# Kernel optimization log

Hardware: AMD Instinct MI355X
Metric: run time of the kernel (lower is better)

Reference implementation:

```python
import jax, jax.numpy as jnp
import numpy as np
from jax import lax

FH, FW = 38, 63          # feature map H,W (600x1000 image, stride 16)
A = 9                    # anchors per location (3 scales x 3 ratios)
POOL = 7                 # cfg.POOLING_SIZE
PRE_NMS, POST_NMS = 6000, 300
NMS_THRESH = 0.7
IM_H, IM_W = 600.0, 1000.0
STRIDE = 16.0


def _make_anchors(h, w, stride=16):
    ratios = np.array([0.5, 1.0, 2.0]); scales = np.array([8.0, 16.0, 32.0])
    base = 16.0; ctr = (base - 1.0) / 2.0
    ws = np.round(np.sqrt(base * base / ratios)); hs = np.round(ws * ratios)
    ws = (ws[:, None] * scales[None, :]).ravel(); hs = (hs[:, None] * scales[None, :]).ravel()
    ba = np.stack([ctr - 0.5 * (ws - 1), ctr - 0.5 * (hs - 1),
                   ctr + 0.5 * (ws - 1), ctr + 0.5 * (hs - 1)], 1)
    sx, sy = np.meshgrid(np.arange(w) * stride, np.arange(h) * stride)
    shifts = np.stack([sx.ravel(), sy.ravel(), sx.ravel(), sy.ravel()], 1)
    return (shifts[:, None, :] + ba[None]).reshape(-1, 4).astype(np.float32)


def _conv(x, w, b, pad):
    y = lax.conv_general_dilated(x, w, (1, 1), pad,
                                 dimension_numbers=('NCHW', 'OIHW', 'NCHW'))
    return y + b[None, :, None, None]


def _bbox_transform_inv(anchors, deltas):
    w = anchors[:, 2] - anchors[:, 0] + 1.0
    h = anchors[:, 3] - anchors[:, 1] + 1.0
    cx = anchors[:, 0] + 0.5 * w
    cy = anchors[:, 1] + 0.5 * h
    dx, dy, dw, dh = deltas[:, 0], deltas[:, 1], deltas[:, 2], deltas[:, 3]
    pcx = dx * w + cx; pcy = dy * h + cy
    pw = jnp.exp(dw) * w; ph = jnp.exp(dh) * h
    return jnp.stack([pcx - 0.5 * pw, pcy - 0.5 * ph,
                      pcx + 0.5 * pw, pcy + 0.5 * ph], 1)


def _nms_keep(boxes, thresh):
    # greedy NMS over score-sorted boxes, fixed-size keep mask
    x1, y1, x2, y2 = boxes[:, 0], boxes[:, 1], boxes[:, 2], boxes[:, 3]
    areas = (x2 - x1 + 1.0) * (y2 - y1 + 1.0)
    iw = jnp.maximum(jnp.minimum(x2[:, None], x2[None, :])
                     - jnp.maximum(x1[:, None], x1[None, :]) + 1.0, 0.0)
    ih = jnp.maximum(jnp.minimum(y2[:, None], y2[None, :])
                     - jnp.maximum(y1[:, None], y1[None, :]) + 1.0, 0.0)
    inter = iw * ih
    iou = inter / (areas[:, None] + areas[None, :] - inter)
    n = boxes.shape[0]; ar = jnp.arange(n)
    def body(i, keep):
        sup = (iou[i] > thresh) & (ar > i) & keep[i]
        return keep & ~sup
    return lax.fori_loop(0, n, body, jnp.ones((n,), bool))


def _crop_and_resize(feat, boxes, crop):
    # feat [C,H,W]; boxes [R,4] normalized (y1,x1,y2,x2); TF crop_and_resize semantics
    C, H, W = feat.shape
    t = jnp.arange(crop, dtype=feat.dtype) / (crop - 1)
    def one(box):
        by1, bx1, by2, bx2 = box
        ys = by1 * (H - 1) + t * (by2 - by1) * (H - 1)
        xs = bx1 * (W - 1) + t * (bx2 - bx1) * (W - 1)
        y0f = jnp.floor(ys); x0f = jnp.floor(xs)
        wy = (ys - y0f)[None, :, None]; wx = (xs - x0f)[None, None, :]
        y0 = jnp.clip(y0f, 0, H - 1).astype(jnp.int32)
        y1i = jnp.clip(y0f + 1, 0, H - 1).astype(jnp.int32)
        x0 = jnp.clip(x0f, 0, W - 1).astype(jnp.int32)
        x1i = jnp.clip(x0f + 1, 0, W - 1).astype(jnp.int32)
        f00 = feat[:, y0][:, :, x0]; f01 = feat[:, y0][:, :, x1i]
        f10 = feat[:, y1i][:, :, x0]; f11 = feat[:, y1i][:, :, x1i]
        return (f00 * (1 - wy) * (1 - wx) + f01 * (1 - wy) * wx
                + f10 * wy * (1 - wx) + f11 * wy * wx)
    return jax.vmap(one)(boxes)


def _forward(net_conv, w_rpn, b_rpn, w_cls, b_cls, w_bbox, b_bbox, anchors):
    # _region_proposal: 3x3 rpn conv + relu, 1x1 cls / bbox heads
    rpn = jax.nn.relu(_conv(net_conv, w_rpn, b_rpn, 'SAME'))
    cls = _conv(rpn, w_cls, b_cls, 'VALID')    # [1,2A,H,W]
    bbox = _conv(rpn, w_bbox, b_bbox, 'VALID')  # [1,4A,H,W]
    # view(1,2,-1,W) softmax: channel a pairs with channel a+A (bg/fg)
    bg, fg = cls[:, :A], cls[:, A:]
    fg_prob = jax.nn.softmax(jnp.stack([bg, fg], axis=1), axis=1)[:, 1]  # [1,A,H,W]
    scores = jnp.transpose(fg_prob, (0, 2, 3, 1)).reshape(-1)            # (H*W*A,)
    deltas = jnp.transpose(bbox, (0, 2, 3, 1)).reshape(-1, 4)
    proposals = _bbox_transform_inv(anchors, deltas)
    proposals = jnp.stack([jnp.clip(proposals[:, 0], 0.0, IM_W - 1.0),
                           jnp.clip(proposals[:, 1], 0.0, IM_H - 1.0),
                           jnp.clip(proposals[:, 2], 0.0, IM_W - 1.0),
                           jnp.clip(proposals[:, 3], 0.0, IM_H - 1.0)], 1)
    # proposal selection is non-differentiable (rois.detach() in original)
    scores_sg = lax.stop_gradient(scores)
    props_sg = lax.stop_gradient(proposals)
    _, order = lax.top_k(scores_sg, PRE_NMS)
    boxes = props_sg[order]
    keep = _nms_keep(boxes, NMS_THRESH)
    idx = jnp.sort(jnp.where(keep, jnp.arange(PRE_NMS), PRE_NMS))[:POST_NMS]
    rois = boxes[jnp.minimum(idx, PRE_NMS - 1)]  # [300,4] (x1,y1,x2,y2)
    # _crop_pool_layer with max_pool=True: crop to 14x14 then 2x2 max pool
    H, W = net_conv.shape[2], net_conv.shape[3]
    x1 = rois[:, 0] / STRIDE; y1 = rois[:, 1] / STRIDE
    x2 = rois[:, 2] / STRIDE; y2 = rois[:, 3] / STRIDE
    norm = jnp.stack([y1 / (H - 1), x1 / (W - 1), y2 / (H - 1), x2 / (W - 1)], 1)
    crops = _crop_and_resize(net_conv[0], norm, 2 * POOL)  # [300,C,14,14]
    R, C = crops.shape[0], crops.shape[1]
    return crops.reshape(R, C, POOL, 2, POOL, 2).max(axis=(3, 5))  # [300,C,7,7]


def setup_inputs():
    key = jax.random.key(0)
    ks = jax.random.split(key, 4)
    net_conv = jax.random.normal(ks[0], (1, 512, FH, FW), jnp.float32)
    w_rpn = jax.random.normal(ks[1], (512, 512, 3, 3), jnp.float32) * 0.01
    b_rpn = jnp.zeros((512,), jnp.float32)
    w_cls = jax.random.normal(ks[2], (2 * A, 512, 1, 1), jnp.float32) * 0.01
    b_cls = jnp.zeros((2 * A,), jnp.float32)
    w_bbox = jax.random.normal(ks[3], (4 * A, 512, 1, 1), jnp.float32) * 0.01
    b_bbox = jnp.zeros((4 * A,), jnp.float32)
    anchors = jnp.asarray(_make_anchors(FH, FW))
    return {"net_conv": net_conv, "w_rpn": w_rpn, "b_rpn": b_rpn,
            "w_cls": w_cls, "b_cls": b_cls, "w_bbox": w_bbox,
            "b_bbox": b_bbox, "anchors": anchors}


def reference(net_conv, w_rpn, b_rpn, w_cls, b_cls, w_bbox, b_bbox, anchors):
    return _forward(net_conv, w_rpn, b_rpn, w_cls, b_cls, w_bbox, b_bbox, anchors)
```

## Files before the change

kernel.cpp:

```cpp
#include <hip/hip_runtime.h>
#include <stdint.h>

#define NPOS 2394
#define CIN 512
#define KK 4608
#define NANCH 21546
#define PRE 6000
#define POST 300
#define NWORD 94
#define NQ 8
#define QLEN 2694
#define FEATT_BYTES 4902912

#define OFF_BH    0
#define OFF_BL    4718592
#define OFF_P0    9437184
#define OFF_SBOX  9437184
#define OFF_KEEP  9533440
#define OFF_P1    14340096
#define OFF_KEYS  19243008
#define OFF_PROP  19415552
#define OFF_RPART 19760384
#define OFF_FPH   20450048
#define OFF_FPL   23179264

typedef _Float16 half8 __attribute__((ext_vector_type(8)));
typedef float f32x4 __attribute__((ext_vector_type(4)));

__device__ __forceinline__ void gload16(const void* g, void* l) {
    __builtin_amdgcn_global_load_lds((const __attribute__((address_space(1))) void*)g,
                                     (__attribute__((address_space(3))) void*)l, 16, 0, 0);
}

__global__ __launch_bounds__(256) void k_transpose_feat(const float* __restrict__ in,
                                                        float* __restrict__ featT) {
    __shared__ float tl[32][33];
    int tx = threadIdx.x & 31, tg = threadIdx.x >> 5;
    int posBase = blockIdx.x * 32, ciBase = blockIdx.y * 32;
#pragma unroll
    for (int j = 0; j < 4; ++j) {
        int ci = ciBase + tg + j * 8;
        int pos = posBase + tx;
        tl[tg + j * 8][tx] = (pos < NPOS) ? in[(size_t)ci * NPOS + pos] : 0.f;
    }
    __syncthreads();
#pragma unroll
    for (int j = 0; j < 4; ++j) {
        int pos = posBase + tg + j * 8;
        int ci = ciBase + tx;
        if (pos < NPOS) featT[(size_t)pos * 512 + ci] = tl[tx][tg + j * 8];
    }
}

__global__ void k_pad_split(const float* __restrict__ featT,
                            _Float16* __restrict__ FPH, _Float16* __restrict__ FPL) {
    int idx = blockIdx.x * 256 + threadIdx.x;
    int ci = idx & 511;
    int rc = idx >> 9;
    int hp = rc / 65, wp = rc - hp * 65;
    int h = hp - 1, w = wp - 1;
    float a = 0.f;
    if ((unsigned)h < 38u && (unsigned)w < 63u)
        a = featT[(size_t)(h * 63 + w) * 512 + ci] * 16.f;
    _Float16 ah = (_Float16)a;
    _Float16 al = (_Float16)(a - (float)ah);
    FPH[idx] = ah; FPL[idx] = al;
}

__global__ void k_prep_wf16(const float* __restrict__ w,
                            _Float16* __restrict__ BH, _Float16* __restrict__ BL) {
    int idx = blockIdx.x * 256 + threadIdx.x;
    int co = idx / KK;
    int rem = idx - co * KK;
    int p = rem >> 9;
    int ci = rem & 511;
    float b = w[(co * CIN + ci) * 9 + p] * 128.f;
    _Float16 bh = (_Float16)b;
    _Float16 bl = (_Float16)(b - (float)bh);
    BH[idx] = bh; BL[idx] = bl;
}

__global__ __launch_bounds__(256, 3) void k_conv3_mfma(
    const _Float16* __restrict__ FPH, const _Float16* __restrict__ FPL,
    const _Float16* __restrict__ BHp, const _Float16* __restrict__ BLp,
    float* __restrict__ P0, float* __restrict__ P1)
{
    __shared__ __align__(16) char lds[49152];
    const int t = threadIdx.x;
    const int wave = t >> 6, lane = t & 63;
    const int posBase = blockIdx.x * 128;
    const int coBase  = blockIdx.y * 64;
    const int z = blockIdx.z;
    float* __restrict__ P = z ? P1 : P0;
    const int wm = wave >> 1, wn = wave & 1;
    const int lr = lane & 15, lg = lane >> 4;

    int addrA[4][2], addrB[2][2];
#pragma unroll
    for (int m = 0; m < 4; ++m) {
        int row = wm * 64 + m * 16 + lr;
        int x = row & 7;
        addrA[m][0] = row * 128 + ((lg ^ x) << 4);
        addrA[m][1] = row * 128 + (((4 + lg) ^ x) << 4);
    }
#pragma unroll
    for (int n = 0; n < 2; ++n) {
        int row = wn * 32 + n * 16 + lr;
        int x = row & 7;
        addrB[n][0] = 32768 + row * 128 + ((lg ^ x) << 4);
        addrB[n][1] = 32768 + row * 128 + (((4 + lg) ^ x) << 4);
    }

    int baseA[4], ldsAo[4];
#pragma unroll
    for (int s = 0; s < 4; ++s) {
        int row = (wave * 4 + s) * 8 + (lane >> 3);
        int pos = posBase + row;
        int h = pos / 63;
        int w = pos - h * 63;
        int swz = ((lane & 7) ^ (row & 7)) * 8;
        baseA[s] = (h * 65 + w) * 512 + swz;
        ldsAo[s] = (wave * 4 + s) * 1024 + lane * 16;
    }
    int baseB[2], ldsBo[2];
#pragma unroll
    for (int s = 0; s < 2; ++s) {
        int row = (wave * 2 + s) * 8 + (lane >> 3);
        int swz = ((lane & 7) ^ (row & 7)) * 8;
        baseB[s] = (coBase + row) * KK + swz;
        ldsBo[s] = 32768 + (wave * 2 + s) * 1024 + lane * 16;
    }

    f32x4 acc[4][2];
#pragma unroll
    for (int m = 0; m < 4; ++m)
#pragma unroll
        for (int n = 0; n < 2; ++n) acc[m][n] = (f32x4){0.f, 0.f, 0.f, 0.f};

    const int kbeg = z * 2304;
    for (int step = 0; step < 36; ++step) {
        int k0 = kbeg + step * 64;
        int p = k0 >> 9;
        int ci0 = k0 & 511;
        int kh = p / 3;
        int kw = p - kh * 3;
        int dA = (kh * 65 + kw) * 512 + ci0;
#pragma unroll
        for (int s = 0; s < 4; ++s) {
            int so = baseA[s] + dA;
            gload16(FPH + so, lds + ldsAo[s]);
            gload16(FPL + so, lds + 16384 + ldsAo[s]);
        }
#pragma unroll
        for (int s = 0; s < 2; ++s) {
            int so = baseB[s] + k0;
            gload16(BHp + so, lds + ldsBo[s]);
            gload16(BLp + so, lds + 8192 + ldsBo[s]);
        }
        __syncthreads();
#pragma unroll
        for (int ks = 0; ks < 2; ++ks) {
            half8 aH[4], aL[4], bH[2], bL[2];
#pragma unroll
            for (int m = 0; m < 4; ++m) {
                aH[m] = *(const half8*)(lds + addrA[m][ks]);
                aL[m] = *(const half8*)(lds + 16384 + addrA[m][ks]);
            }
#pragma unroll
            for (int n = 0; n < 2; ++n) {
                bH[n] = *(const half8*)(lds + addrB[n][ks]);
                bL[n] = *(const half8*)(lds + 8192 + addrB[n][ks]);
            }
#pragma unroll
            for (int m = 0; m < 4; ++m)
#pragma unroll
                for (int n = 0; n < 2; ++n) {
                    acc[m][n] = __builtin_amdgcn_mfma_f32_16x16x32_f16(aH[m], bH[n], acc[m][n], 0, 0, 0);
                    acc[m][n] = __builtin_amdgcn_mfma_f32_16x16x32_f16(aH[m], bL[n], acc[m][n], 0, 0, 0);
                    acc[m][n] = __builtin_amdgcn_mfma_f32_16x16x32_f16(aL[m], bH[n], acc[m][n], 0, 0, 0);
                }
        }
        __syncthreads();
    }

#pragma unroll
    for (int m = 0; m < 4; ++m) {
        int pbase = posBase + wm * 64 + m * 16 + lg * 4;
        int co = coBase + wn * 32 + lr;
#pragma unroll
        for (int r = 0; r < 4; ++r) {
            int pos = pbase + r;
            if (pos < NPOS) {
                P[(size_t)pos * 512 + co]      = acc[m][0][r] * (1.f / 2048.f);
                P[(size_t)pos * 512 + co + 16] = acc[m][1][r] * (1.f / 2048.f);
            }
        }
    }
}

__global__ __launch_bounds__(256) void k_heads(const float* __restrict__ P0,
                                               const float* __restrict__ P1,
                                               const float* __restrict__ brpn,
                                               const float* __restrict__ wcls,
                                               const float* __restrict__ bcls,
                                               const float* __restrict__ wbbox,
                                               const float* __restrict__ bbbox,
                                               const float* __restrict__ anchors,
                                               float* __restrict__ proposals,
                                               unsigned long long* __restrict__ keys) {
    __shared__ float x[512];
    __shared__ float part[54][4];
    __shared__ float logit[54];
    int pos = blockIdx.x;
    int t = threadIdx.x;
    {
        float v0 = P0[(size_t)pos * 512 + t] + P1[(size_t)pos * 512 + t] + brpn[t];
        float v1 = P0[(size_t)pos * 512 + t + 256] + P1[(size_t)pos * 512 + t + 256] + brpn[t + 256];
        x[t] = v0 > 0.f ? v0 : 0.f;
        x[t + 256] = v1 > 0.f ? v1 : 0.f;
    }
    __syncthreads();
    if (t < 216) {
        int o = t >> 2, q = t & 3;
        const float* wr = (o < 18) ? (wcls + o * 512) : (wbbox + (o - 18) * 512);
        float s = 0.f;
        int base = q * 128;
#pragma unroll 4
        for (int k2 = 0; k2 < 128; ++k2) s += x[base + k2] * wr[base + k2];
        part[o][q] = s;
    }
    __syncthreads();
    if (t < 54) {
        float b = (t < 18) ? bcls[t] : bbbox[t - 18];
        logit[t] = part[t][0] + part[t][1] + part[t][2] + part[t][3] + b;
    }
    __syncthreads();
    if (t < 9) {
        int a = t;
        float bg = logit[a], fg = logit[9 + a];
        float score = 1.f / (1.f + expf(bg - fg));
        float dx = logit[18 + 4 * a], dy = logit[19 + 4 * a];
        float dw = logit[20 + 4 * a], dh = logit[21 + 4 * a];
        int idx = pos * 9 + a;
        float ax1 = anchors[idx * 4 + 0], ay1 = anchors[idx * 4 + 1];
        float ax2 = anchors[idx * 4 + 2], ay2 = anchors[idx * 4 + 3];
        float aw = ax2 - ax1 + 1.f, ah = ay2 - ay1 + 1.f;
        float cx = ax1 + 0.5f * aw, cy = ay1 + 0.5f * ah;
        float pcx = dx * aw + cx, pcy = dy * ah + cy;
        float pw = expf(dw) * aw, ph = expf(dh) * ah;
        float x1 = fminf(fmaxf(pcx - 0.5f * pw, 0.f), 999.f);
        float y1 = fminf(fmaxf(pcy - 0.5f * ph, 0.f), 599.f);
        float x2 = fminf(fmaxf(pcx + 0.5f * pw, 0.f), 999.f);
        float y2 = fminf(fmaxf(pcy + 0.5f * ph, 0.f), 599.f);
        proposals[idx * 4 + 0] = x1; proposals[idx * 4 + 1] = y1;
        proposals[idx * 4 + 2] = x2; proposals[idx * 4 + 3] = y2;
        union { float f; unsigned int i; } sv; sv.f = score;
        keys[idx] = (((unsigned long long)sv.i) << 32) |
                    (unsigned long long)(0xFFFFFFFFu - (unsigned)idx);
    }
}

__global__ __launch_bounds__(256) void k_rank_partial(const unsigned long long* __restrict__ keys,
                                                      unsigned int* __restrict__ rpart) {
    __shared__ unsigned long long kc[1024];
    int i = blockIdx.x * 256 + threadIdx.x;
    int q = blockIdx.y;
    unsigned long long myk = (i < NANCH) ? keys[i] : 0xFFFFFFFFFFFFFFFFull;
    int j0 = q * QLEN;
    int j1 = j0 + QLEN; if (j1 > NANCH) j1 = NANCH;
    unsigned int cnt = 0;
    for (int base = j0; base < j1; base += 1024) {
        int nload = j1 - base; if (nload > 1024) nload = 1024;
        __syncthreads();
        for (int u = threadIdx.x; u < 1024; u += 256)
            kc[u] = (base + u < j1) ? keys[base + u] : 0ull;
        __syncthreads();
        for (int u = 0; u < nload; ++u)
            cnt += (kc[u] > myk) ? 1u : 0u;
    }
    if (i < NANCH) rpart[i * NQ + q] = cnt;
}

__global__ void k_zero_sboxes(float* __restrict__ sboxes) {
    int i = blockIdx.x * 256 + threadIdx.x;
    if (i < PRE * 4) sboxes[i] = 0.f;
}

__global__ void k_rank_scatter(const unsigned int* __restrict__ rpart,
                               const float* __restrict__ proposals,
                               float* __restrict__ sboxes) {
    int i = blockIdx.x * 256 + threadIdx.x;
    if (i >= NANCH) return;
    unsigned int r = 0;
#pragma unroll
    for (int q = 0; q < NQ; q++) r += rpart[i * NQ + q];
    if (r < PRE) {
        sboxes[r * 4 + 0] = proposals[i * 4 + 0];
        sboxes[r * 4 + 1] = proposals[i * 4 + 1];
        sboxes[r * 4 + 2] = proposals[i * 4 + 2];
        sboxes[r * 4 + 3] = proposals[i * 4 + 3];
    }
}

__global__ __launch_bounds__(64) void k_nms_mask(const float* __restrict__ sboxes,
                                                 unsigned long long* __restrict__ mask) {
    __shared__ float bx[64][4];
    int ib = blockIdx.x, jb = blockIdx.y;
    int lane = threadIdx.x;
    int j = jb * 64 + lane;
    if (j < PRE) {
        bx[lane][0] = sboxes[j * 4 + 0]; bx[lane][1] = sboxes[j * 4 + 1];
        bx[lane][2] = sboxes[j * 4 + 2]; bx[lane][3] = sboxes[j * 4 + 3];
    } else {
        bx[lane][0] = 3e8f; bx[lane][1] = 3e8f; bx[lane][2] = 3e8f; bx[lane][3] = 3e8f;
    }
    __syncthreads();
    int i = ib * 64 + lane;
    if (i >= PRE) return;
    float x1 = sboxes[i * 4 + 0], y1 = sboxes[i * 4 + 1];
    float x2 = sboxes[i * 4 + 2], y2 = sboxes[i * 4 + 3];
    float ar = (x2 - x1 + 1.f) * (y2 - y1 + 1.f);
    unsigned long long bits = 0;
#pragma unroll 4
    for (int u = 0; u < 64; u++) {
        int j2 = jb * 64 + u;
        float iw = fminf(x2, bx[u][2]) - fmaxf(x1, bx[u][0]) + 1.f;
        float ih = fminf(y2, bx[u][3]) - fmaxf(y1, bx[u][1]) + 1.f;
        iw = fmaxf(iw, 0.f); ih = fmaxf(ih, 0.f);
        float inter = iw * ih;
        float arj = (bx[u][2] - bx[u][0] + 1.f) * (bx[u][3] - bx[u][1] + 1.f);
        float iou = inter / (ar + arj - inter);
        if (iou > 0.7f && j2 > i) bits |= (1ull << u);
    }
    mask[(size_t)i * NWORD + jb] = bits;
}

__global__ __launch_bounds__(64) void k_nms_scan(const unsigned long long* __restrict__ mask,
                                                 int* __restrict__ keep) {
    int lane = threadIdx.x;
    unsigned long long rem0 = 0, rem1 = 0;
    int nk = 0;
    for (int b = 0; b < NWORD && nk < POST; ++b) {
        unsigned long long rm = (b < 64) ? __shfl(rem0, b) : __shfl(rem1, b - 64);
        unsigned long long valid = (b == NWORD - 1) ? ((1ull << 48) - 1) : ~0ull;
        unsigned long long alive = ~rm & valid;
        while (alive) {
            int u = __ffsll((long long)alive) - 1;
            int i = b * 64 + u;
            if (lane == 0) keep[nk] = i;
            ++nk;
            if (nk == POST) break;
            const unsigned long long* row = mask + (size_t)i * NWORD;
            rem0 |= row[lane];
            if (lane < NWORD - 64) rem1 |= row[64 + lane];
            unsigned long long rmb = (b < 64) ? __shfl(rem0, b) : __shfl(rem1, b - 64);
            unsigned long long above = (u == 63) ? 0ull : (~0ull << (u + 1));
            alive = ~rmb & valid & above;
        }
    }
    for (int k2 = nk + lane; k2 < POST; k2 += 64) keep[k2] = PRE - 1;
}

__global__ __launch_bounds__(256) void k_gather_rois(const float* sboxes, const int* keep,
                                                     float* outF) {
    int t = threadIdx.x;
    float4 box[2];
    int nr = 0;
    for (int r = t; r < POST; r += 256) {
        int ki = keep[r];
        if (ki < 0) ki = 0; if (ki > PRE - 1) ki = PRE - 1;
        box[nr++] = *reinterpret_cast<const float4*>(sboxes + ki * 4);
    }
    __syncthreads();
    nr = 0;
    for (int r = t; r < POST; r += 256) {
        float4 b = box[nr++];
#pragma unroll
        for (int cg = 0; cg < 8; ++cg)
            *reinterpret_cast<float4*>(outF + (size_t)(r * 512 + cg * 64) * 49) = b;
    }
}

__global__ __launch_bounds__(256) void k_crop_fast(const float* __restrict__ featT,
                                                   float* out) {
    __shared__ float lds[4][49 * 65];
    int r = blockIdx.x;
    int w = threadIdx.x >> 6, lane = threadIdx.x & 63;
    int cg = blockIdx.y * 4 + w;
    int c = cg * 64 + lane;
    float* chunk = out + (size_t)(r * 512 + cg * 64) * 49;
    const float4 b = *reinterpret_cast<const float4*>(chunk);
    float x1 = b.x, y1 = b.y, x2 = b.z, y2 = b.w;
    float by1 = (y1 / 16.f) / 37.f, bx1 = (x1 / 16.f) / 62.f;
    float by2 = (y2 / 16.f) / 37.f, bx2 = (x2 / 16.f) / 62.f;
    float dyn = by2 - by1, dxn = bx2 - bx1;
    for (int e = 0; e < 49; ++e) {
        int oy = e / 7, ox = e - oy * 7;
        float vv[4];
#pragma unroll
        for (int dy = 0; dy < 2; ++dy) {
            int sy = 2 * oy + dy;
            float ty = (float)sy / 13.f;
            float ys = by1 * 37.f + (ty * dyn) * 37.f;
            float yf = floorf(ys);
            float wy = ys - yf;
            int y0  = (int)fminf(fmaxf(yf, 0.f), 37.f);
            int y1i = (int)fminf(fmaxf(yf + 1.f, 0.f), 37.f);
#pragma unroll
            for (int dxx = 0; dxx < 2; ++dxx) {
                int sx = 2 * ox + dxx;
                float tx = (float)sx / 13.f;
                float xs = bx1 * 62.f + (tx * dxn) * 62.f;
                float xf = floorf(xs);
                float wx = xs - xf;
                int x0  = (int)fminf(fmaxf(xf, 0.f), 62.f);
                int x1i = (int)fminf(fmaxf(xf + 1.f, 0.f), 62.f);
                float f00 = featT[(size_t)(y0 * 63 + x0) * 512 + c];
                float f01 = featT[(size_t)(y0 * 63 + x1i) * 512 + c];
                float f10 = featT[(size_t)(y1i * 63 + x0) * 512 + c];
                float f11 = featT[(size_t)(y1i * 63 + x1i) * 512 + c];
                vv[dy * 2 + dxx] = f00 * (1.f - wy) * (1.f - wx) + f01 * (1.f - wy) * wx +
                                   f10 * wy * (1.f - wx) + f11 * wy * wx;
            }
        }
        lds[w][e * 65 + lane] = fmaxf(fmaxf(vv[0], vv[1]), fmaxf(vv[2], vv[3]));
    }
    __syncthreads();
    for (int i = lane; i < 64 * 49; i += 64) {
        int cl = i / 49, e = i - cl * 49;
        chunk[i] = lds[w][e * 65 + cl];
    }
}

__global__ __launch_bounds__(64) void k_crop_slow(const float* __restrict__ net,
                                                  float* out) {
    int r = blockIdx.x, cg = blockIdx.y;
    int lane = threadIdx.x;
    int c = cg * 64 + lane;
    const float4 b = *reinterpret_cast<const float4*>(out + (size_t)(r * 512 + cg * 64) * 49);
    float x1 = b.x, y1 = b.y, x2 = b.z, y2 = b.w;
    float by1 = (y1 / 16.f) / 37.f, bx1 = (x1 / 16.f) / 62.f;
    float by2 = (y2 / 16.f) / 37.f, bx2 = (x2 / 16.f) / 62.f;
    float dyn = by2 - by1, dxn = bx2 - bx1;
    const float* fc = net + (size_t)c * NPOS;
    float* orow = out + ((size_t)r * 512 + c) * 49;
    for (int e = 0; e < 49; ++e) {
        int oy = e / 7, ox = e - oy * 7;
        float vv[4];
#pragma unroll
        for (int dy = 0; dy < 2; ++dy) {
            int sy = 2 * oy + dy;
            float ty = (float)sy / 13.f;
            float ys = by1 * 37.f + (ty * dyn) * 37.f;
            float yf = floorf(ys);
            float wy = ys - yf;
            int y0  = (int)fminf(fmaxf(yf, 0.f), 37.f);
            int y1i = (int)fminf(fmaxf(yf + 1.f, 0.f), 37.f);
#pragma unroll
            for (int dxx = 0; dxx < 2; ++dxx) {
                int sx = 2 * ox + dxx;
                float tx = (float)sx / 13.f;
                float xs = bx1 * 62.f + (tx * dxn) * 62.f;
                float xf = floorf(xs);
                float wx = xs - xf;
                int x0  = (int)fminf(fmaxf(xf, 0.f), 62.f);
                int x1i = (int)fminf(fmaxf(xf + 1.f, 0.f), 62.f);
                float f00 = fc[y0 * 63 + x0];
                float f01 = fc[y0 * 63 + x1i];
                float f10 = fc[y1i * 63 + x0];
                float f11 = fc[y1i * 63 + x1i];
                vv[dy * 2 + dxx] = f00 * (1.f - wy) * (1.f - wx) + f01 * (1.f - wy) * wx +
                                   f10 * wy * (1.f - wx) + f11 * wy * wx;
            }
        }
        orow[e] = fmaxf(fmaxf(vv[0], vv[1]), fmaxf(vv[2], vv[3]));
    }
}

extern "C" void kernel_launch(void* const* d_in, const int* in_sizes, int n_in,
                              void* d_out, int out_size, void* d_ws, size_t ws_size,
                              hipStream_t stream) {
    auto find = [&](int count, int fallback) {
        for (int i = 0; i < n_in; ++i) if (in_sizes[i] == count) return i;
        return fallback;
    };
    const float* net   = (const float*)d_in[find(NPOS * CIN, 0)];
    const float* wrpn  = (const float*)d_in[find(512 * KK, 1)];
    const float* brpn  = (const float*)d_in[find(512, 2)];
    const float* wcls  = (const float*)d_in[find(18 * 512, 3)];
    const float* bcls  = (const float*)d_in[find(18, 4)];
    const float* wbbox = (const float*)d_in[find(36 * 512, 5)];
    const float* bbbox = (const float*)d_in[find(36, 6)];
    const float* anch  = (const float*)d_in[find(NANCH * 4, 7)];

    char* ob = (char*)d_out;
    _Float16* BH             = (_Float16*)(ob + OFF_BH);
    _Float16* BL             = (_Float16*)(ob + OFF_BL);
    unsigned long long* mask = (unsigned long long*)(ob + OFF_BH);
    float* P0                = (float*)(ob + OFF_P0);
    float* P1                = (float*)(ob + OFF_P1);
    float* sboxes            = (float*)(ob + OFF_SBOX);
    int* keep                = (int*)(ob + OFF_KEEP);
    unsigned long long* keys = (unsigned long long*)(ob + OFF_KEYS);
    float* proposals         = (float*)(ob + OFF_PROP);
    unsigned int* rpart      = (unsigned int*)(ob + OFF_RPART);
    _Float16* FPH            = (_Float16*)(ob + OFF_FPH);
    _Float16* FPL            = (_Float16*)(ob + OFF_FPL);
    float* outF              = (float*)d_out;

    const bool ws_ok = (ws_size >= (size_t)FEATT_BYTES);
    float* featT = ws_ok ? (float*)d_ws : (float*)(ob + OFF_P0);

    hipLaunchKernelGGL(k_transpose_feat, dim3(75, 16), dim3(256), 0, stream, net, featT);
    hipLaunchKernelGGL(k_pad_split, dim3(5330), dim3(256), 0, stream, featT, FPH, FPL);
    hipLaunchKernelGGL(k_prep_wf16, dim3(9216), dim3(256), 0, stream, wrpn, BH, BL);
    hipLaunchKernelGGL(k_conv3_mfma, dim3(19, 8, 2), dim3(256), 0, stream, FPH, FPL, BH, BL, P0, P1);
    hipLaunchKernelGGL(k_heads, dim3(NPOS), dim3(256), 0, stream, P0, P1, brpn, wcls, bcls, wbbox, bbbox, anch, proposals, keys);
    hipLaunchKernelGGL(k_rank_partial, dim3(85, NQ), dim3(256), 0, stream, keys, rpart);
    hipLaunchKernelGGL(k_zero_sboxes, dim3((PRE * 4 + 255) / 256), dim3(256), 0, stream, sboxes);
    hipLaunchKernelGGL(k_rank_scatter, dim3(85), dim3(256), 0, stream, rpart, proposals, sboxes);
    hipLaunchKernelGGL(k_nms_mask, dim3(NWORD, NWORD), dim3(64), 0, stream, sboxes, mask);
    hipLaunchKernelGGL(k_nms_scan, dim3(1), dim3(64), 0, stream, mask, keep);
    hipLaunchKernelGGL(k_gather_rois, dim3(1), dim3(256), 0, stream, sboxes, keep, outF);
    if (ws_ok)
        hipLaunchKernelGGL(k_crop_fast, dim3(POST, 2), dim3(256), 0, stream, featT, outF);
    else
        hipLaunchKernelGGL(k_crop_slow, dim3(POST, 8), dim3(64), 0, stream, net, outF);
}
```

Measured before the change: 466.2 us.

## Double-buffer NMS mask rows into LDS windows for the serial scan

The single-wave NMS scan now runs with four waves that cooperatively prefetch 32-row windows of the suppression mask into double-buffered LDS using async global-to-LDS loads. The serial greedy walk then reads each kept row from LDS instead of global memory, hiding the dependent global load latency on the critical path. The cost is a barrier per 32-row window, even when no box in that window survives. It relies on the mask row stride of 752 bytes and padded LDS rows, and gload16 is assumed to be defined elsewhere.

```diff
diff --git a/kernel.cpp b/kernel.cpp
--- a/kernel.cpp
+++ b/kernel.cpp
@@ -335,30 +335,78 @@
     mask[(size_t)i * NWORD + jb] = bits;
 }
 
-__global__ __launch_bounds__(64) void k_nms_scan(const unsigned long long* __restrict__ mask,
-                                                 int* __restrict__ keep) {
-    int lane = threadIdx.x;
+#define NMSW 32
+#define NWIN 188
+#define ROWPAD 768
+#define WINB (NMSW * ROWPAD)
+__global__ __launch_bounds__(256) void k_nms_scan(const unsigned long long* __restrict__ mask,
+                                                  int* __restrict__ keep) {
+    __shared__ __align__(16) char ldsw[2 * WINB];
+    const int t = threadIdx.x, wave = t >> 6, lane = t & 63;
+    const char* mb = (const char*)mask;
+
+    const char* src[6];
+    int ldso[6];
+#pragma unroll
+    for (int k = 0; k < 6; ++k) {
+        int g = (wave * 6 + k) * 64 + lane;
+        int row = g / 48, off = g - row * 48;
+        src[k] = mb + (size_t)row * 752 + off * 16;
+        ldso[k] = (wave * 6 + k) * 1024;
+    }
+
+#pragma unroll
+    for (int k = 0; k < 6; ++k) gload16(src[k], ldsw + ldso[k]);
+    asm volatile("s_waitcnt vmcnt(0)" ::: "memory");
+    __builtin_amdgcn_s_barrier();
+    asm volatile("" ::: "memory");
+
     unsigned long long rem0 = 0, rem1 = 0;
     int nk = 0;
-    for (int b = 0; b < NWORD && nk < POST; ++b) {
-        unsigned long long rm = (b < 64) ? __shfl(rem0, b) : __shfl(rem1, b - 64);
-        unsigned long long valid = (b == NWORD - 1) ? ((1ull << 48) - 1) : ~0ull;
-        unsigned long long alive = ~rm & valid;
-        while (alive) {
-            int u = __ffsll((long long)alive) - 1;
-            int i = b * 64 + u;
-            if (lane == 0) keep[nk] = i;
-            ++nk;
-            if (nk == POST) break;
-            const unsigned long long* row = mask + (size_t)i * NWORD;
-            rem0 |= row[lane];
-            if (lane < NWORD - 64) rem1 |= row[64 + lane];
-            unsigned long long rmb = (b < 64) ? __shfl(rem0, b) : __shfl(rem1, b - 64);
-            unsigned long long above = (u == 63) ? 0ull : (~0ull << (u + 1));
-            alive = ~rmb & valid & above;
-        }
-    }
-    for (int k2 = nk + lane; k2 < POST; k2 += 64) keep[k2] = PRE - 1;
+    for (int w = 0; w < NWIN; ++w) {
+        int cb = w & 1;
+        if (w + 1 < NWIN) {
+#pragma unroll
+            for (int k = 0; k < 6; ++k)
+                gload16(src[k] + (size_t)(w + 1) * (NMSW * 752), ldsw + (cb ^ 1) * WINB + ldso[k]);
+            asm volatile("s_waitcnt vmcnt(6)" ::: "memory");
+        } else {
+            asm volatile("s_waitcnt vmcnt(0)" ::: "memory");
+        }
+        __builtin_amdgcn_s_barrier();
+        asm volatile("" ::: "memory");
+
+        {
+            int b = w >> 1;
+            unsigned long long valid = (b == NWORD - 1) ? ((1ull << 48) - 1) : ~0ull;
+            unsigned long long wmask = (w & 1) ? 0xFFFFFFFF00000000ull : 0x00000000FFFFFFFFull;
+            unsigned long long rm = (b < 64) ? __shfl(rem0, b) : __shfl(rem1, b - 64);
+            unsigned long long alive = ~rm & valid & wmask;
+            const char* basep = ldsw + cb * WINB;
+            while (alive) {
+                int u = __ffsll((long long)alive) - 1;
+                int i = b * 64 + u;
+                if (wave == 0 && lane == 0) keep[nk] = i;
+                ++nk;
+                if (nk == POST) break;
+                const unsigned long long* lrow =
+                    (const unsigned long long*)(basep + (i - w * NMSW) * ROWPAD);
+                unsigned long long w0 = lrow[lane];
+                unsigned long long w1 = 0;
+                if (lane < NWORD - 64) w1 = lrow[64 + lane];
+                rem0 |= w0; rem1 |= w1;
+                rm = (b < 64) ? __shfl(rem0, b) : __shfl(rem1, b - 64);
+                alive = ~rm & valid & wmask & ((u == 63) ? 0ull : (~0ull << (u + 1)));
+            }
+        }
+        if (nk >= POST) break;
+        asm volatile("" ::: "memory");
+        __builtin_amdgcn_s_barrier();
+        asm volatile("" ::: "memory");
+    }
+    asm volatile("s_waitcnt vmcnt(0)" ::: "memory");
+    if (wave == 0)
+        for (int k2 = nk + lane; k2 < POST; k2 += 64) keep[k2] = PRE - 1;
 }
 
 __global__ __launch_bounds__(256) void k_gather_rois(const float* sboxes, const int* keep,
@@ -520,7 +568,7 @@
     hipLaunchKernelGGL(k_zero_sboxes, dim3((PRE * 4 + 255) / 256), dim3(256), 0, stream, sboxes);
     hipLaunchKernelGGL(k_rank_scatter, dim3(85), dim3(256), 0, stream, rpart, proposals, sboxes);
     hipLaunchKernelGGL(k_nms_mask, dim3(NWORD, NWORD), dim3(64), 0, stream, sboxes, mask);
-    hipLaunchKernelGGL(k_nms_scan, dim3(1), dim3(64), 0, stream, mask, keep);
+    hipLaunchKernelGGL(k_nms_scan, dim3(1), dim3(64 * 4), 0, stream, mask, keep);
     hipLaunchKernelGGL(k_gather_rois, dim3(1), dim3(256), 0, stream, sboxes, keep, outF);
     if (ws_ok)
         hipLaunchKernelGGL(k_crop_fast, dim3(POST, 2), dim3(256), 0, stream, featT, outF);
```

New measurement: 426.8 us. -8.4%, faster.

## Restructure NMS scan to use LDS-resident diagonal blocks and batched row merges

Applied to the files above, without the earlier changes.

The mask kernel now also writes the 128x128 diagonal super-block bits to a separate compact buffer, and stores the full mask with nontemporal stores. The single-wave scan kernel preloads all diagonal blocks into LDS and resolves kept boxes within each 128-box super-block using shuffles of LDS data instead of dependent global row loads. Suppression rows for kept boxes are then OR-merged from global memory in batches of eight, so the loads are independent rather than serialized per kept box. This is meant to cut the latency-bound serial chain in greedy NMS, at the cost of about 94 KB of LDS and extra diagonal stores.

```diff
diff --git a/kernel.cpp b/kernel.cpp
--- a/kernel.cpp
+++ b/kernel.cpp
@@ -17,6 +17,7 @@
 #define OFF_P0    9437184
 #define OFF_SBOX  9437184
 #define OFF_KEEP  9533440
+#define OFF_DIAG  9633792
 #define OFF_P1    14340096
 #define OFF_KEYS  19243008
 #define OFF_PROP  19415552
@@ -303,7 +304,8 @@
 }
 
 __global__ __launch_bounds__(64) void k_nms_mask(const float* __restrict__ sboxes,
-                                                 unsigned long long* __restrict__ mask) {
+                                                 unsigned long long* __restrict__ mask,
+                                                 unsigned long long* __restrict__ diag2) {
     __shared__ float bx[64][4];
     int ib = blockIdx.x, jb = blockIdx.y;
     int lane = threadIdx.x;
@@ -332,30 +334,84 @@
         float iou = inter / (ar + arj - inter);
         if (iou > 0.7f && j2 > i) bits |= (1ull << u);
     }
-    mask[(size_t)i * NWORD + jb] = bits;
+    __builtin_nontemporal_store(bits, &mask[(size_t)i * NWORD + jb]);
+    if ((ib >> 1) == (jb >> 1)) diag2[(size_t)i * 2 + (jb & 1)] = bits;
 }
 
 __global__ __launch_bounds__(64) void k_nms_scan(const unsigned long long* __restrict__ mask,
+                                                 const unsigned long long* __restrict__ diag2,
                                                  int* __restrict__ keep) {
-    int lane = threadIdx.x;
+    __shared__ __align__(16) unsigned long long ldsd[12032];
+    const int lane = threadIdx.x;
+
+    {
+        const char* g = (const char*)diag2;
+        char* l = (char*)ldsd;
+        for (int r = 0; r < 94; ++r)
+            gload16(g + r * 1024 + (size_t)lane * 16, l + r * 1024);
+        asm volatile("s_waitcnt vmcnt(0)" ::: "memory");
+    }
+
     unsigned long long rem0 = 0, rem1 = 0;
     int nk = 0;
-    for (int b = 0; b < NWORD && nk < POST; ++b) {
-        unsigned long long rm = (b < 64) ? __shfl(rem0, b) : __shfl(rem1, b - 64);
-        unsigned long long valid = (b == NWORD - 1) ? ((1ull << 48) - 1) : ~0ull;
-        unsigned long long alive = ~rm & valid;
-        while (alive) {
-            int u = __ffsll((long long)alive) - 1;
-            int i = b * 64 + u;
-            if (lane == 0) keep[nk] = i;
-            ++nk;
-            if (nk == POST) break;
-            const unsigned long long* row = mask + (size_t)i * NWORD;
-            rem0 |= row[lane];
-            if (lane < NWORD - 64) rem1 |= row[64 + lane];
-            unsigned long long rmb = (b < 64) ? __shfl(rem0, b) : __shfl(rem1, b - 64);
-            unsigned long long above = (u == 63) ? 0ull : (~0ull << (u + 1));
-            alive = ~rmb & valid & above;
+
+    for (int sb = 0; sb < 47; ++sb) {
+        const int w0 = 2 * sb;
+        const int base = sb * 128;
+        ulonglong2 lo = *reinterpret_cast<const ulonglong2*>(&ldsd[(size_t)(base + lane) * 2]);
+        unsigned long long c1b = ldsd[(size_t)(base + 64 + lane) * 2 + 1];
+
+        unsigned long long rm0 = (w0 < 64) ? __shfl(rem0, w0) : __shfl(rem1, w0 - 64);
+        unsigned long long rm1 = (w0 + 1 < 64) ? __shfl(rem0, w0 + 1) : __shfl(rem1, w0 - 63);
+        const unsigned long long valid1 = (sb == 46) ? ((1ull << 48) - 1) : ~0ull;
+        unsigned long long above0 = ~0ull, above1 = ~0ull;
+        unsigned long long keptLo = 0, keptHi = 0;
+
+        for (;;) {
+            unsigned long long a0 = ~rm0 & above0;
+            if (a0) {
+                int u = __ffsll((long long)a0) - 1;
+                if (lane == 0) keep[nk] = base + u;
+                ++nk; if (nk == POST) break;
+                rm0 |= __shfl(lo.x, u);
+                rm1 |= __shfl(lo.y, u);
+                above0 = (u == 63) ? 0ull : (~0ull << (u + 1));
+                keptLo |= 1ull << u;
+                continue;
+            }
+            unsigned long long a1 = ~rm1 & valid1 & above1;
+            if (a1) {
+                int u = __ffsll((long long)a1) - 1;
+                if (lane == 0) keep[nk] = base + 64 + u;
+                ++nk; if (nk == POST) break;
+                rm1 |= __shfl(c1b, u);
+                above1 = (u == 63) ? 0ull : (~0ull << (u + 1));
+                keptHi |= 1ull << u;
+                continue;
+            }
+            break;
+        }
+        if (nk >= POST) break;
+
+        while (keptLo | keptHi) {
+            int j[8];
+#pragma unroll
+            for (int q = 0; q < 8; ++q) {
+                int jj = -1;
+                if (keptLo)      { int u = __ffsll((long long)keptLo) - 1; keptLo &= keptLo - 1; jj = base + u; }
+                else if (keptHi) { int u = __ffsll((long long)keptHi) - 1; keptHi &= keptHi - 1; jj = base + 64 + u; }
+                j[q] = jj;
+            }
+#pragma unroll
+            for (int q = 1; q < 8; ++q) if (j[q] < 0) j[q] = j[0];
+            unsigned long long a0 = 0, a1 = 0;
+#pragma unroll
+            for (int q = 0; q < 8; ++q) {
+                const unsigned long long* r = mask + (size_t)j[q] * NWORD;
+                a0 |= r[lane];
+                if (lane < NWORD - 64) a1 |= r[64 + lane];
+            }
+            rem0 |= a0; rem1 |= a1;
         }
     }
     for (int k2 = nk + lane; k2 < POST; k2 += 64) keep[k2] = PRE - 1;
@@ -501,6 +557,7 @@
     float* P1                = (float*)(ob + OFF_P1);
     float* sboxes            = (float*)(ob + OFF_SBOX);
     int* keep                = (int*)(ob + OFF_KEEP);
+    unsigned long long* diag2= (unsigned long long*)(ob + OFF_DIAG);
     unsigned long long* keys = (unsigned long long*)(ob + OFF_KEYS);
     float* proposals         = (float*)(ob + OFF_PROP);
     unsigned int* rpart      = (unsigned int*)(ob + OFF_RPART);
@@ -519,8 +576,8 @@
     hipLaunchKernelGGL(k_rank_partial, dim3(85, NQ), dim3(256), 0, stream, keys, rpart);
     hipLaunchKernelGGL(k_zero_sboxes, dim3((PRE * 4 + 255) / 256), dim3(256), 0, stream, sboxes);
     hipLaunchKernelGGL(k_rank_scatter, dim3(85), dim3(256), 0, stream, rpart, proposals, sboxes);
-    hipLaunchKernelGGL(k_nms_mask, dim3(NWORD, NWORD), dim3(64), 0, stream, sboxes, mask);
-    hipLaunchKernelGGL(k_nms_scan, dim3(1), dim3(64), 0, stream, mask, keep);
+    hipLaunchKernelGGL(k_nms_mask, dim3(NWORD, NWORD), dim3(64), 0, stream, sboxes, mask, diag2);
+    hipLaunchKernelGGL(k_nms_scan, dim3(1), dim3(64), 0, stream, mask, diag2, keep);
     hipLaunchKernelGGL(k_gather_rois, dim3(1), dim3(256), 0, stream, sboxes, keep, outF);
     if (ws_ok)
         hipLaunchKernelGGL(k_crop_fast, dim3(POST, 2), dim3(256), 0, stream, featT, outF);
```

After: 524.0 us. +12.4%, slower.
